# Optimization experiments

Hardware: AMD Instinct MI355X
Metric: run time of the kernel (lower is better)

The kernel has to match this reference:

```python
import jax, jax.numpy as jnp
import numpy as np

N_NODES = 100000
N_EDGES = 3200000
IN_DIM = 128
HID = 16
MEM = 16
N_LAYERS = 2
OUT = 2
SLOPE = 0.01  # torch leaky_relu default negative_slope


def setup_inputs() -> dict:
    key = jax.random.key(0)
    ks = jax.random.split(key, 20)
    s = 0.05
    inp = {
        "x": jax.random.normal(ks[0], (N_NODES, IN_DIM), dtype=jnp.float32),
        "edge_index": jax.random.randint(ks[1], (2, N_EDGES), 0, N_NODES, dtype=jnp.int64),
        # preprocess MLP: Linear(input_dim,256) -> Linear(256,hidden)
        "pre1_W": jax.random.normal(ks[2], (256, IN_DIM), dtype=jnp.float32) * s,
        "pre1_b": jax.random.normal(ks[3], (256,), dtype=jnp.float32) * s,
        "pre2_W": jax.random.normal(ks[4], (HID, 256), dtype=jnp.float32) * s,
        "pre2_b": jax.random.normal(ks[5], (HID,), dtype=jnp.float32) * s,
        # per-layer hypernetwork GRU biases (input & initial hidden are zeros, so
        # only biases affect the GRU step) and weight_transform Linear(mem, hid*hid)
        "gru_bih": jax.random.normal(ks[6], (N_LAYERS, 3 * MEM), dtype=jnp.float32) * s,
        "gru_bhh": jax.random.normal(ks[7], (N_LAYERS, 3 * MEM), dtype=jnp.float32) * s,
        "wt_W": jax.random.normal(ks[8], (N_LAYERS, HID * HID, MEM), dtype=jnp.float32) * s,
        "wt_b": jax.random.normal(ks[9], (N_LAYERS, HID * HID), dtype=jnp.float32) * s,
        # GCNConv bias (kept as its own parameter in PyG; lin has bias=False)
        "gcn_b": jax.random.normal(ks[10], (N_LAYERS, HID), dtype=jnp.float32) * s,
        # postprocess heads
        "post1_W": jax.random.normal(ks[11], (OUT, HID), dtype=jnp.float32) * s,
        "post1_b": jax.random.normal(ks[12], (OUT,), dtype=jnp.float32) * s,
        "posta_W": jax.random.normal(ks[13], (1, HID), dtype=jnp.float32) * s,
        "posta_b": jax.random.normal(ks[14], (1,), dtype=jnp.float32) * s,
    }
    return inp


def _hyper_gcn_weight(bih, bhh, wt_W, wt_b):
    # GRU single step with zero input and zero initial hidden state:
    # only the biases contribute.  h' = (1-z)*n + z*h_prev, h_prev = 0.
    r = jax.nn.sigmoid(bih[:MEM] + bhh[:MEM])
    z = jax.nn.sigmoid(bih[MEM:2 * MEM] + bhh[MEM:2 * MEM])
    n = jnp.tanh(bih[2 * MEM:] + r * bhh[2 * MEM:])
    mem = (1.0 - z) * n  # [MEM]
    # weight_transform Linear -> view as lin.weight [out, in]; detached in torch
    W = (wt_W @ mem + wt_b).reshape(HID, HID)
    return jax.lax.stop_gradient(W)


def reference(x, edge_index, pre1_W, pre1_b, pre2_W, pre2_b, gru_bih, gru_bhh,
              wt_W, wt_b, gcn_b, post1_W, post1_b, posta_W, posta_b):
    N = x.shape[0]
    # preprocess (dropout p=0.0 -> identity)
    h = jax.nn.leaky_relu(x @ pre1_W.T + pre1_b, negative_slope=SLOPE)
    h = jax.nn.leaky_relu(h @ pre2_W.T + pre2_b, negative_slope=SLOPE)

    # GCN normalization with self-loops (PyG gcn_norm)
    src, dst = edge_index[0], edge_index[1]
    loops = jnp.arange(N, dtype=src.dtype)
    s = jnp.concatenate([src, loops])
    d = jnp.concatenate([dst, loops])
    deg = jax.ops.segment_sum(jnp.ones_like(d, dtype=h.dtype), d, num_segments=N)
    dinv = jnp.where(deg > 0, jax.lax.rsqrt(deg), 0.0)
    norm = dinv[s] * dinv[d]  # [E+N]

    for l in range(N_LAYERS):
        W = _hyper_gcn_weight(gru_bih[l], gru_bhh[l], wt_W[l], wt_b[l])
        xw = h @ W.T                                   # [N, HID]
        msg = xw[s] * norm[:, None]                    # gather + scale
        h = jax.ops.segment_sum(msg, d, num_segments=N) + gcn_b[l]
        h = jax.nn.leaky_relu(h, negative_slope=SLOPE)

    out = jnp.sum(h @ post1_W.T + post1_b, axis=-1)          # [N]
    anomaly = (h @ posta_W.T + posta_b)[:, 0]                # [N]
    return out, anomaly, h
```

## Files before the change

### kernel.cpp

```cpp
#include <hip/hip_runtime.h>
#include <hip/hip_bf16.h>
#include <math.h>

#define IN_DIM 128
#define PRE_HID 256
#define HID 16

__device__ __forceinline__ float lrelu(float v) { return v > 0.f ? v : 0.01f * v; }
__device__ __forceinline__ float fin(float v) { return (v == v && fabsf(v) < 1e30f) ? v : 0.f; }

__device__ __forceinline__ float ldp(const void* p, size_t i, int f32) {
    if (f32) return ((const float*)p)[i];
    unsigned u = ((const unsigned short*)p)[i];
    return __uint_as_float(u << 16);
}
__device__ __forceinline__ unsigned short f2bf(float f) {
    union { __hip_bfloat16 b; unsigned short u; } cv;
    cv.b = __float2bfloat16(f);
    return cv.u;
}
__device__ __forceinline__ void unpack8(uint4 u, float* o) {
    o[0] = __uint_as_float(u.x << 16); o[1] = __uint_as_float(u.x & 0xFFFF0000u);
    o[2] = __uint_as_float(u.y << 16); o[3] = __uint_as_float(u.y & 0xFFFF0000u);
    o[4] = __uint_as_float(u.z << 16); o[5] = __uint_as_float(u.z & 0xFFFF0000u);
    o[6] = __uint_as_float(u.w << 16); o[7] = __uint_as_float(u.w & 0xFFFF0000u);
}
__device__ __forceinline__ unsigned pk2(float a, float b) {
    return (unsigned)f2bf(a) | ((unsigned)f2bf(b) << 16);
}
__device__ __forceinline__ uint4 pack8(const float* v) {
    uint4 u;
    u.x = pk2(v[0], v[1]); u.y = pk2(v[2], v[3]);
    u.z = pk2(v[4], v[5]); u.w = pk2(v[6], v[7]);
    return u;
}

#define OFF_W1F   0
#define OFF_B1F   32768
#define OFF_W2T   33024
#define OFF_B2F   37120
#define OFF_HW    37136
#define OFF_GCNB  37648
#define OFF_POST  37680
#define OFF_FLAGS 37720
#define OFF_BSUM  37760
#define OFF_BPRE  37888
#define OFF_A0    38016

__global__ void k_detect(const unsigned short* __restrict__ xu,
                         const int* __restrict__ ei32, int* __restrict__ flags) {
    if (threadIdx.x == 0 && blockIdx.x == 0) {
        int band = 0;
        for (int k = 0; k < 128; ++k) {
            unsigned e = (xu[2 * k] >> 7) & 0xFF;
            if (e >= 100 && e <= 140) band++;
        }
        flags[1] = (band < 96) ? 1 : 0;
        int any = 0;
        for (int k = 0; k < 64; ++k) any |= ei32[2 * k + 1];
        flags[0] = (any == 0) ? 1 : 0;
    }
}

__global__ void k_sentinel(unsigned* __restrict__ out, int words, unsigned val) {
    int i = blockIdx.x * 256 + threadIdx.x;
    if (i < words) out[i] = val;
}

__global__ void k_prep_small(const void* __restrict__ bih, const void* __restrict__ bhh,
                             const void* __restrict__ wtW, const void* __restrict__ wtb,
                             const void* __restrict__ p1W, const void* __restrict__ p1b,
                             const void* __restrict__ paW, const void* __restrict__ pab,
                             const int* __restrict__ flags,
                             float* __restrict__ hw, float* __restrict__ post) {
    int f32 = flags[1];
    __shared__ float mem[2][16];
    int t = threadIdx.x;
    if (t < 32) {
        int l = t >> 4, j = t & 15;
        float bi0 = ldp(bih, l * 48 + j, f32),      bh0 = ldp(bhh, l * 48 + j, f32);
        float bi1 = ldp(bih, l * 48 + 16 + j, f32), bh1 = ldp(bhh, l * 48 + 16 + j, f32);
        float bi2 = ldp(bih, l * 48 + 32 + j, f32), bh2 = ldp(bhh, l * 48 + 32 + j, f32);
        float r = 1.f / (1.f + expf(-(bi0 + bh0)));
        float z = 1.f / (1.f + expf(-(bi1 + bh1)));
        float nn = tanhf(bi2 + r * bh2);
        mem[l][j] = (1.f - z) * nn;
    }
    __syncthreads();
    for (int l = 0; l < 2; ++l) {
        float acc = ldp(wtb, l * 256 + t, f32);
        #pragma unroll
        for (int m = 0; m < 16; ++m)
            acc += ldp(wtW, l * 4096 + t * 16 + m, f32) * mem[l][m];
        hw[l * 256 + t] = acc;
    }
    if (t < 16) {
        post[t]      = ldp(p1W, t, f32) + ldp(p1W, 16 + t, f32);
        post[17 + t] = ldp(paW, t, f32);
    }
    if (t == 0) {
        post[16] = ldp(p1b, 0, f32) + ldp(p1b, 1, f32);
        post[33] = ldp(pab, 0, f32);
    }
}

__global__ void k_convert(const void* __restrict__ p1W, const void* __restrict__ p1b,
                          const void* __restrict__ p2W, const void* __restrict__ p2b,
                          const void* __restrict__ gcnb, const int* __restrict__ flags,
                          float* __restrict__ w1f, float* __restrict__ b1f,
                          float* __restrict__ w2t, float* __restrict__ b2f,
                          float* __restrict__ gcnbf) {
    int f32 = flags[1];
    int i = blockIdx.x * 256 + threadIdx.x;
    if (i < 32768) w1f[i] = ldp(p1W, i, f32);
    if (i < 256)   b1f[i] = ldp(p1b, i, f32);
    if (i < 4096)  { int r = i >> 4, j = i & 15; w2t[i] = ldp(p2W, j * 256 + r, f32); }
    if (i < 16)    b2f[i] = ldp(p2b, i, f32);
    if (i < 32)    gcnbf[i] = ldp(gcnb, i, f32);
}

__global__ void k_deg(const int* __restrict__ ei, const int* __restrict__ flags,
                      unsigned* __restrict__ deg, int E, int N) {
    int e = blockIdx.x * 256 + threadIdx.x;
    if (e >= E) return;
    int d = flags[0] ? ei[2 * ((size_t)E + e)] : ei[(size_t)E + e];
    if ((unsigned)d < (unsigned)N) atomicAdd(&deg[d], 1u);
}

__global__ void k_dinv(float* __restrict__ degdinv, int N) {
    int n = blockIdx.x * 256 + threadIdx.x;
    if (n >= N) return;
    unsigned dg = ((unsigned*)degdinv)[n];
    degdinv[n] = 1.f / sqrtf((float)dg + 1.f);
}

__global__ void k_dinv2(const unsigned* __restrict__ deg, float* __restrict__ dinv, int N) {
    int n = blockIdx.x * 256 + threadIdx.x;
    if (n >= N) return;
    dinv[n] = 1.f / sqrtf((float)deg[n] + 1.f);
}

__global__ __launch_bounds__(1024) void k_scan_block(const unsigned* __restrict__ deg,
                                                     unsigned* __restrict__ bsum, int N) {
    __shared__ unsigned s[1024];
    int t = threadIdx.x;
    int i = blockIdx.x * 1024 + t;
    s[t] = (i < N) ? deg[i] : 0u;
    __syncthreads();
    for (int off = 512; off > 0; off >>= 1) {
        if (t < off) s[t] += s[t + off];
        __syncthreads();
    }
    if (t == 0) bsum[blockIdx.x] = s[0];
}

__global__ __launch_bounds__(128) void k_scan_top(unsigned* __restrict__ bsum,
                                                  unsigned* __restrict__ bpre, int NB) {
    __shared__ unsigned s[128];
    int t = threadIdx.x;
    unsigned v = (t < NB) ? bsum[t] : 0u;
    s[t] = v;
    __syncthreads();
    for (int off = 1; off < 128; off <<= 1) {
        unsigned a = (t >= off) ? s[t - off] : 0u;
        __syncthreads();
        s[t] += a;
        __syncthreads();
    }
    if (t < NB) bpre[t] = s[t] - v;
}

__global__ __launch_bounds__(1024) void k_scan_final(const unsigned* __restrict__ deg,
                                                     const unsigned* __restrict__ bpre,
                                                     unsigned* __restrict__ rowptr, int N) {
    __shared__ unsigned s[1024];
    int t = threadIdx.x;
    int i = blockIdx.x * 1024 + t;
    unsigned v = (i < N) ? deg[i] : 0u;
    s[t] = v;
    __syncthreads();
    for (int off = 1; off < 1024; off <<= 1) {
        unsigned a = (t >= off) ? s[t - off] : 0u;
        __syncthreads();
        s[t] += a;
        __syncthreads();
    }
    if (i < N) rowptr[i] = bpre[blockIdx.x] + s[t] - v;
}

__global__ void k_fill(const int* __restrict__ ei, const int* __restrict__ flags,
                       unsigned* __restrict__ rowptr, unsigned* __restrict__ csr,
                       int E, int N) {
    int e = blockIdx.x * 256 + threadIdx.x;
    if (e >= E) return;
    int s, d;
    if (flags[0]) { s = ei[2 * (size_t)e]; d = ei[2 * ((size_t)E + e)]; }
    else          { s = ei[e];             d = ei[(size_t)E + e]; }
    if ((unsigned)d >= (unsigned)N) return;
    if ((unsigned)s >= (unsigned)N) s = d;
    unsigned pos = atomicAdd(&rowptr[d], 1u);
    csr[pos] = (unsigned)s;
}

__global__ __launch_bounds__(256) void k_pre(const void* __restrict__ x,
                                             const float* __restrict__ w1f,
                                             const float* __restrict__ b1f,
                                             const float* __restrict__ w2t,
                                             const float* __restrict__ b2f,
                                             const int* __restrict__ flags,
                                             float* __restrict__ h, int N) {
    int n = blockIdx.x * 256 + threadIdx.x;
    if (n >= N) return;
    float xr[IN_DIM];
    if (flags[1]) {
        const float4* xp = reinterpret_cast<const float4*>((const float*)x + (size_t)n * IN_DIM);
        #pragma unroll
        for (int i = 0; i < 32; ++i) {
            float4 v = xp[i];
            xr[i * 4 + 0] = v.x; xr[i * 4 + 1] = v.y; xr[i * 4 + 2] = v.z; xr[i * 4 + 3] = v.w;
        }
    } else {
        const uint4* xp = reinterpret_cast<const uint4*>((const unsigned short*)x + (size_t)n * IN_DIM);
        #pragma unroll
        for (int i = 0; i < 16; ++i) unpack8(xp[i], xr + i * 8);
    }
    float acc2[HID];
    #pragma unroll
    for (int j = 0; j < HID; ++j) acc2[j] = b2f[j];
    for (int r = 0; r < PRE_HID; ++r) {
        float s = b1f[r];
        const float* wr = w1f + r * IN_DIM;
        #pragma unroll
        for (int k = 0; k < IN_DIM; ++k) s += wr[k] * xr[k];
        s = lrelu(s);
        const float* w2r = w2t + r * HID;
        #pragma unroll
        for (int j = 0; j < HID; ++j) acc2[j] += w2r[j] * s;
    }
    float4* hp = reinterpret_cast<float4*>(h + (size_t)n * HID);
    #pragma unroll
    for (int q = 0; q < 4; ++q) {
        float4 v;
        v.x = lrelu(acc2[q * 4 + 0]); v.y = lrelu(acc2[q * 4 + 1]);
        v.z = lrelu(acc2[q * 4 + 2]); v.w = lrelu(acc2[q * 4 + 3]);
        hp[q] = v;
    }
}

__global__ void k_xw_y(const float* __restrict__ h, const float* __restrict__ W,
                       const float* __restrict__ dinv, float* __restrict__ y, int N) {
    int n = blockIdx.x * 256 + threadIdx.x;
    if (n >= N) return;
    float hv[HID];
    const float4* hp = reinterpret_cast<const float4*>(h + (size_t)n * HID);
    #pragma unroll
    for (int q = 0; q < 4; ++q) {
        float4 v = hp[q];
        hv[q*4+0] = v.x; hv[q*4+1] = v.y; hv[q*4+2] = v.z; hv[q*4+3] = v.w;
    }
    float dn = dinv[n];
    float4* yp = reinterpret_cast<float4*>(y + (size_t)n * HID);
    #pragma unroll
    for (int q = 0; q < 4; ++q) {
        float o[4];
        #pragma unroll
        for (int ii = 0; ii < 4; ++ii) {
            int i = q * 4 + ii;
            float s = 0.f;
            #pragma unroll
            for (int j = 0; j < HID; ++j) s += W[i * HID + j] * hv[j];
            o[ii] = s * dn;
        }
        float4 v; v.x = o[0]; v.y = o[1]; v.z = o[2]; v.w = o[3];
        yp[q] = v;
    }
}

__global__ __launch_bounds__(256) void k_gather(const unsigned* __restrict__ rowptr,
                                                const unsigned* __restrict__ deg,
                                                const unsigned* __restrict__ csr,
                                                const float* __restrict__ y,
                                                const float* __restrict__ dinv,
                                                const float* __restrict__ gcnbf,
                                                float* __restrict__ h, int N) {
    int tid = blockIdx.x * 256 + threadIdx.x;
    if (tid >= N * HID) return;
    int n = tid >> 4, f = tid & 15;
    unsigned end = rowptr[n];
    unsigned start = end - deg[n];
    float acc = y[(size_t)n * HID + f];
    for (unsigned k = start; k < end; ++k) {
        unsigned src = csr[k];
        acc += y[(size_t)src * HID + f];
    }
    h[(size_t)n * HID + f] = lrelu(fin(dinv[n] * acc) + gcnbf[f]);
}

__global__ __launch_bounds__(256) void k_gather_final(const unsigned* __restrict__ rowptr,
                                                      const unsigned* __restrict__ deg,
                                                      const unsigned* __restrict__ csr,
                                                      const float* __restrict__ y,
                                                      const float* __restrict__ dinv,
                                                      const float* __restrict__ gcnbf,
                                                      const float* __restrict__ post,
                                                      const int* __restrict__ flags,
                                                      void* __restrict__ out, int N) {
    int tid = blockIdx.x * 256 + threadIdx.x;
    if (tid >= N * HID) return;
    int n = tid >> 4, f = tid & 15;
    unsigned end = rowptr[n];
    unsigned start = end - deg[n];
    float acc = y[(size_t)n * HID + f];
    for (unsigned k = start; k < end; ++k) {
        unsigned src = csr[k];
        acc += y[(size_t)src * HID + f];
    }
    float v = lrelu(fin(dinv[n] * acc) + gcnbf[f]);
    float s1 = v * post[f];
    float s2 = v * post[17 + f];
    #pragma unroll
    for (int m = 1; m < 16; m <<= 1) {
        s1 += __shfl_xor(s1, m, 64);
        s2 += __shfl_xor(s2, m, 64);
    }
    if (flags[1]) {
        float* ob = (float*)out;
        if (f == 0) ob[n] = s1 + post[16];
        if (f == 1) ob[N + n] = s2 + post[33];
        ob[2 * (size_t)N + (size_t)n * HID + f] = v;
    } else {
        unsigned short* ob = (unsigned short*)out;
        if (f == 0) ob[n] = f2bf(s1 + post[16]);
        if (f == 1) ob[N + n] = f2bf(s2 + post[33]);
        ob[2 * (size_t)N + (size_t)n * HID + f] = f2bf(v);
    }
}

__global__ void k_xw(const float* __restrict__ h, const float* __restrict__ W,
                     const float* __restrict__ dinv, const int* __restrict__ flags,
                     void* __restrict__ xw, float* __restrict__ hacc, int N) {
    int n = blockIdx.x * 256 + threadIdx.x;
    if (n >= N) return;
    float hv[HID];
    const float4* hp = reinterpret_cast<const float4*>(h + (size_t)n * HID);
    #pragma unroll
    for (int q = 0; q < 4; ++q) {
        float4 v = hp[q];
        hv[q*4+0] = v.x; hv[q*4+1] = v.y; hv[q*4+2] = v.z; hv[q*4+3] = v.w;
    }
    float dn = dinv[n];
    float sl = dn * dn;
    float o[HID];
    #pragma unroll
    for (int i = 0; i < HID; ++i) {
        float s = 0.f;
        #pragma unroll
        for (int j = 0; j < HID; ++j) s += W[i * HID + j] * hv[j];
        o[i] = s;
    }
    if (flags[1]) {
        float4* xp = reinterpret_cast<float4*>((float*)xw + (size_t)n * HID);
        #pragma unroll
        for (int q = 0; q < 4; ++q) {
            float4 v; v.x = o[q*4+0]; v.y = o[q*4+1]; v.z = o[q*4+2]; v.w = o[q*4+3];
            xp[q] = v;
        }
    } else {
        uint4* xp = reinterpret_cast<uint4*>((unsigned short*)xw + (size_t)n * HID);
        xp[0] = pack8(o);
        xp[1] = pack8(o + 8);
    }
    float4* ap = reinterpret_cast<float4*>(hacc + (size_t)n * HID);
    #pragma unroll
    for (int q = 0; q < 4; ++q) {
        float4 va;
        va.x = o[q*4+0]*sl; va.y = o[q*4+1]*sl; va.z = o[q*4+2]*sl; va.w = o[q*4+3]*sl;
        ap[q] = va;
    }
}

__global__ __launch_bounds__(256) void k_scatter(const int* __restrict__ ei,
                                                 const int* __restrict__ flags,
                                                 const float* __restrict__ dinv,
                                                 const void* __restrict__ xw,
                                                 float* __restrict__ hacc, int E, int N) {
    int e = blockIdx.x * 256 + threadIdx.x;
    if (e >= E) return;
    int s, d;
    if (flags[0]) { s = ei[2 * (size_t)e]; d = ei[2 * ((size_t)E + e)]; }
    else          { s = ei[e];             d = ei[(size_t)E + e]; }
    if ((unsigned)s >= (unsigned)N || (unsigned)d >= (unsigned)N) return;
    float nrm = dinv[s] * dinv[d];
    float v[HID];
    if (flags[1]) {
        const float4* xr = reinterpret_cast<const float4*>((const float*)xw + (size_t)s * HID);
        #pragma unroll
        for (int q = 0; q < 4; ++q) {
            float4 a = xr[q];
            v[q*4+0] = a.x; v[q*4+1] = a.y; v[q*4+2] = a.z; v[q*4+3] = a.w;
        }
    } else {
        const uint4* xr = reinterpret_cast<const uint4*>((const unsigned short*)xw + (size_t)s * HID);
        unpack8(xr[0], v);
        unpack8(xr[1], v + 8);
    }
    float* out = hacc + (size_t)d * HID;
    #pragma unroll
    for (int j = 0; j < HID; ++j) unsafeAtomicAdd(out + j, v[j] * nrm);
}

__global__ void k_finish(const float* __restrict__ hacc, const float* __restrict__ gcnbf,
                         float* __restrict__ h, int N) {
    int n = blockIdx.x * 256 + threadIdx.x;
    if (n >= N) return;
    const float4* ap = reinterpret_cast<const float4*>(hacc + (size_t)n * HID);
    float4* hp = reinterpret_cast<float4*>(h + (size_t)n * HID);
    #pragma unroll
    for (int q = 0; q < 4; ++q) {
        float4 a = ap[q];
        float4 o;
        o.x = lrelu(fin(a.x) + gcnbf[q*4+0]);
        o.y = lrelu(fin(a.y) + gcnbf[q*4+1]);
        o.z = lrelu(fin(a.z) + gcnbf[q*4+2]);
        o.w = lrelu(fin(a.w) + gcnbf[q*4+3]);
        hp[q] = o;
    }
}

__global__ void k_final(const float* __restrict__ hacc, const float* __restrict__ gcnbf,
                        const float* __restrict__ post, const int* __restrict__ flags,
                        void* __restrict__ out, int N) {
    int n = blockIdx.x * 256 + threadIdx.x;
    if (n >= N) return;
    float v[HID];
    const float4* ap = reinterpret_cast<const float4*>(hacc + (size_t)n * HID);
    #pragma unroll
    for (int q = 0; q < 4; ++q) {
        float4 a = ap[q];
        v[q*4+0] = lrelu(fin(a.x) + gcnbf[q*4+0]);
        v[q*4+1] = lrelu(fin(a.y) + gcnbf[q*4+1]);
        v[q*4+2] = lrelu(fin(a.z) + gcnbf[q*4+2]);
        v[q*4+3] = lrelu(fin(a.w) + gcnbf[q*4+3]);
    }
    float o = post[16], an = post[33];
    #pragma unroll
    for (int j = 0; j < HID; ++j) {
        o += v[j] * post[j];
        an += v[j] * post[17 + j];
    }
    if (flags[1]) {
        float* ob = (float*)out;
        ob[n] = o;
        ob[N + n] = an;
        float* hr = ob + 2 * (size_t)N + (size_t)n * HID;
        #pragma unroll
        for (int j = 0; j < HID; ++j) hr[j] = v[j];
    } else {
        unsigned short* ob = (unsigned short*)out;
        ob[n] = f2bf(o);
        ob[N + n] = f2bf(an);
        uint4* hr = reinterpret_cast<uint4*>(ob + 2 * (size_t)N + (size_t)n * HID);
        hr[0] = pack8(v);
        hr[1] = pack8(v + 8);
    }
}

extern "C" void kernel_launch(void* const* d_in, const int* in_sizes, int n_in,
                              void* d_out, int out_size, void* d_ws, size_t ws_size,
                              hipStream_t stream) {
    const void* x    = d_in[0];
    const int*  ei   = (const int*)d_in[1];
    const void* p1W  = d_in[2];
    const void* p1b  = d_in[3];
    const void* p2W  = d_in[4];
    const void* p2b  = d_in[5];
    const void* bih  = d_in[6];
    const void* bhh  = d_in[7];
    const void* wtW  = d_in[8];
    const void* wtb  = d_in[9];
    const void* gcnb = d_in[10];
    const void* po1W = d_in[11];
    const void* po1b = d_in[12];
    const void* poaW = d_in[13];
    const void* poab = d_in[14];

    const int N = in_sizes[0] / IN_DIM;
    const int E = in_sizes[1] / 2;

    float* ws = (float*)d_ws;
    float* w1f   = ws + OFF_W1F;
    float* b1f   = ws + OFF_B1F;
    float* w2t   = ws + OFF_W2T;
    float* b2f   = ws + OFF_B2F;
    float* hw    = ws + OFF_HW;
    float* gcnbf = ws + OFF_GCNB;
    float* post  = ws + OFF_POST;
    int*   flags = (int*)(ws + OFF_FLAGS);
    unsigned* bsum = (unsigned*)(ws + OFF_BSUM);
    unsigned* bpre = (unsigned*)(ws + OFF_BPRE);

    const int nb_nodes = (N + 255) / 256;
    const int nb_edges = (E + 255) / 256;
    const int nb_nf    = (N * HID + 255) / 256;
    const int NB       = (N + 1023) / 1024;

    size_t req_csr = ((size_t)OFF_A0 + 35 * (size_t)N + (size_t)E + 64) * 4;
    size_t req_fb  = ((size_t)OFF_A0 + 33 * (size_t)N + 64) * 4;

    if (ws_size >= req_csr && NB <= 128) {
        unsigned* deg    = (unsigned*)(ws + OFF_A0);
        unsigned* rowptr = deg + N;
        float*    dinv   = (float*)(rowptr + N);
        unsigned* csr    = (unsigned*)(dinv + N);
        float*    y      = (float*)(csr + E);
        float*    h      = y + (size_t)N * HID;

        hipMemsetAsync(deg, 0, (size_t)N * 4, stream);
        k_detect<<<1, 64, 0, stream>>>((const unsigned short*)x, ei, flags);
        k_prep_small<<<1, 256, 0, stream>>>(bih, bhh, wtW, wtb, po1W, po1b, poaW, poab,
                                            flags, hw, post);
        k_convert<<<128, 256, 0, stream>>>(p1W, p1b, p2W, p2b, gcnb, flags,
                                           w1f, b1f, w2t, b2f, gcnbf);
        k_deg<<<nb_edges, 256, 0, stream>>>(ei, flags, deg, E, N);
        k_dinv2<<<nb_nodes, 256, 0, stream>>>(deg, dinv, N);
        k_scan_block<<<NB, 1024, 0, stream>>>(deg, bsum, N);
        k_scan_top<<<1, 128, 0, stream>>>(bsum, bpre, NB);
        k_scan_final<<<NB, 1024, 0, stream>>>(deg, bpre, rowptr, N);
        k_fill<<<nb_edges, 256, 0, stream>>>(ei, flags, rowptr, csr, E, N);
        k_pre<<<nb_nodes, 256, 0, stream>>>(x, w1f, b1f, w2t, b2f, flags, h, N);

        k_xw_y<<<nb_nodes, 256, 0, stream>>>(h, hw + 0, dinv, y, N);
        k_gather<<<nb_nf, 256, 0, stream>>>(rowptr, deg, csr, y, dinv, gcnbf + 0, h, N);
        k_xw_y<<<nb_nodes, 256, 0, stream>>>(h, hw + 256, dinv, y, N);
        k_gather_final<<<nb_nf, 256, 0, stream>>>(rowptr, deg, csr, y, dinv, gcnbf + 16,
                                                  post, flags, d_out, N);
    } else if (ws_size >= req_fb) {
        float* degdinv = ws + OFF_A0;
        float* hacc    = degdinv + N;
        float* h       = hacc + (size_t)N * HID;
        void*  xw      = d_out;

        hipMemsetAsync(degdinv, 0, (size_t)N * 4, stream);
        k_detect<<<1, 64, 0, stream>>>((const unsigned short*)x, ei, flags);
        k_prep_small<<<1, 256, 0, stream>>>(bih, bhh, wtW, wtb, po1W, po1b, poaW, poab,
                                            flags, hw, post);
        k_convert<<<128, 256, 0, stream>>>(p1W, p1b, p2W, p2b, gcnb, flags,
                                           w1f, b1f, w2t, b2f, gcnbf);
        k_deg<<<nb_edges, 256, 0, stream>>>(ei, flags, (unsigned*)degdinv, E, N);
        k_dinv<<<nb_nodes, 256, 0, stream>>>(degdinv, N);
        k_pre<<<nb_nodes, 256, 0, stream>>>(x, w1f, b1f, w2t, b2f, flags, h, N);
        for (int l = 0; l < 2; ++l) {
            k_xw<<<nb_nodes, 256, 0, stream>>>(h, hw + l * 256, degdinv, flags, xw, hacc, N);
            k_scatter<<<nb_edges, 256, 0, stream>>>(ei, flags, degdinv, xw, hacc, E, N);
            if (l == 0) k_finish<<<nb_nodes, 256, 0, stream>>>(hacc, gcnbf + 0, h, N);
            else        k_final<<<nb_nodes, 256, 0, stream>>>(hacc, gcnbf + 16, post, flags, d_out, N);
        }
    } else {
        float f = 256.0f + (float)(ws_size >> 20);
        unsigned uv; __builtin_memcpy(&uv, &f, 4);
        int words = out_size / 2;
        k_sentinel<<<(words + 255) / 256, 256, 0, stream>>>((unsigned*)d_out, words, uv);
    }
}
```

Before: 1.085 ms.

## Tile preprocess MLP over hidden rows and vectorize CSR gathers with float4

The preprocess kernel no longer holds a 128-float input row in registers. It walks 32-row tiles of the first layer and streams the input in chunks of 8, keeping 32 partial sums, which is meant to cut register pressure and raise occupancy. The gather kernels now use 4 threads per node, each loading float4 slices, instead of 16 scalar threads. This cuts per-edge loads of CSR indices and row pointers by a factor of four but gives fewer threads per node. The input is now re-read 8 times from cache in the preprocess kernel.

```diff
diff --git a/kernel.cpp b/kernel.cpp
--- a/kernel.cpp
+++ b/kernel.cpp
@@ -211,31 +211,45 @@
                                              float* __restrict__ h, int N) {
     int n = blockIdx.x * 256 + threadIdx.x;
     if (n >= N) return;
-    float xr[IN_DIM];
-    if (flags[1]) {
-        const float4* xp = reinterpret_cast<const float4*>((const float*)x + (size_t)n * IN_DIM);
-        #pragma unroll
-        for (int i = 0; i < 32; ++i) {
-            float4 v = xp[i];
-            xr[i * 4 + 0] = v.x; xr[i * 4 + 1] = v.y; xr[i * 4 + 2] = v.z; xr[i * 4 + 3] = v.w;
-        }
-    } else {
-        const uint4* xp = reinterpret_cast<const uint4*>((const unsigned short*)x + (size_t)n * IN_DIM);
-        #pragma unroll
-        for (int i = 0; i < 16; ++i) unpack8(xp[i], xr + i * 8);
-    }
+    const int f32 = flags[1];
+    const float* xf = (const float*)x + (size_t)n * IN_DIM;
+    const unsigned short* xb = (const unsigned short*)x + (size_t)n * IN_DIM;
+
     float acc2[HID];
     #pragma unroll
     for (int j = 0; j < HID; ++j) acc2[j] = b2f[j];
-    for (int r = 0; r < PRE_HID; ++r) {
-        float s = b1f[r];
-        const float* wr = w1f + r * IN_DIM;
-        #pragma unroll
-        for (int k = 0; k < IN_DIM; ++k) s += wr[k] * xr[k];
-        s = lrelu(s);
-        const float* w2r = w2t + r * HID;
-        #pragma unroll
-        for (int j = 0; j < HID; ++j) acc2[j] += w2r[j] * s;
+
+    for (int rt = 0; rt < 8; ++rt) {
+        float s[32];
+        #pragma unroll
+        for (int r = 0; r < 32; ++r) s[r] = b1f[rt * 32 + r];
+        for (int kc = 0; kc < 16; ++kc) {
+            float xr[8];
+            if (f32) {
+                float4 a = *reinterpret_cast<const float4*>(xf + kc * 8);
+                float4 b = *reinterpret_cast<const float4*>(xf + kc * 8 + 4);
+                xr[0] = a.x; xr[1] = a.y; xr[2] = a.z; xr[3] = a.w;
+                xr[4] = b.x; xr[5] = b.y; xr[6] = b.z; xr[7] = b.w;
+            } else {
+                uint4 u = *reinterpret_cast<const uint4*>(xb + kc * 8);
+                unpack8(u, xr);
+            }
+            const float* wbase = w1f + (size_t)(rt * 32) * IN_DIM + kc * 8;
+            #pragma unroll
+            for (int r = 0; r < 32; ++r) {
+                const float* wr = wbase + (size_t)r * IN_DIM;
+                #pragma unroll
+                for (int k = 0; k < 8; ++k) s[r] += wr[k] * xr[k];
+            }
+        }
+        const float* w2base = w2t + (size_t)(rt * 32) * HID;
+        #pragma unroll
+        for (int r = 0; r < 32; ++r) {
+            float t = lrelu(s[r]);
+            const float* w2r = w2base + (size_t)r * HID;
+            #pragma unroll
+            for (int j = 0; j < HID; ++j) acc2[j] += w2r[j] * t;
+        }
     }
     float4* hp = reinterpret_cast<float4*>(h + (size_t)n * HID);
     #pragma unroll
@@ -284,16 +298,23 @@
                                                 const float* __restrict__ gcnbf,
                                                 float* __restrict__ h, int N) {
     int tid = blockIdx.x * 256 + threadIdx.x;
-    if (tid >= N * HID) return;
-    int n = tid >> 4, f = tid & 15;
+    if (tid >= N * 4) return;
+    int n = tid >> 2, q = tid & 3;
     unsigned end = rowptr[n];
     unsigned start = end - deg[n];
-    float acc = y[(size_t)n * HID + f];
+    float4 acc = *reinterpret_cast<const float4*>(y + (size_t)n * HID + q * 4);
     for (unsigned k = start; k < end; ++k) {
         unsigned src = csr[k];
-        acc += y[(size_t)src * HID + f];
-    }
-    h[(size_t)n * HID + f] = lrelu(fin(dinv[n] * acc) + gcnbf[f]);
+        float4 v = *reinterpret_cast<const float4*>(y + (size_t)src * HID + q * 4);
+        acc.x += v.x; acc.y += v.y; acc.z += v.z; acc.w += v.w;
+    }
+    float dn = dinv[n];
+    float4 o;
+    o.x = lrelu(fin(dn * acc.x) + gcnbf[q*4+0]);
+    o.y = lrelu(fin(dn * acc.y) + gcnbf[q*4+1]);
+    o.z = lrelu(fin(dn * acc.z) + gcnbf[q*4+2]);
+    o.w = lrelu(fin(dn * acc.w) + gcnbf[q*4+3]);
+    *reinterpret_cast<float4*>(h + (size_t)n * HID + q * 4) = o;
 }
 
 __global__ __launch_bounds__(256) void k_gather_final(const unsigned* __restrict__ rowptr,
@@ -306,33 +327,40 @@
                                                       const int* __restrict__ flags,
                                                       void* __restrict__ out, int N) {
     int tid = blockIdx.x * 256 + threadIdx.x;
-    if (tid >= N * HID) return;
-    int n = tid >> 4, f = tid & 15;
+    if (tid >= N * 4) return;
+    int n = tid >> 2, q = tid & 3;
     unsigned end = rowptr[n];
     unsigned start = end - deg[n];
-    float acc = y[(size_t)n * HID + f];
+    float4 acc = *reinterpret_cast<const float4*>(y + (size_t)n * HID + q * 4);
     for (unsigned k = start; k < end; ++k) {
         unsigned src = csr[k];
-        acc += y[(size_t)src * HID + f];
-    }
-    float v = lrelu(fin(dinv[n] * acc) + gcnbf[f]);
-    float s1 = v * post[f];
-    float s2 = v * post[17 + f];
-    #pragma unroll
-    for (int m = 1; m < 16; m <<= 1) {
+        float4 v = *reinterpret_cast<const float4*>(y + (size_t)src * HID + q * 4);
+        acc.x += v.x; acc.y += v.y; acc.z += v.z; acc.w += v.w;
+    }
+    float dn = dinv[n];
+    float v0 = lrelu(fin(dn * acc.x) + gcnbf[q*4+0]);
+    float v1 = lrelu(fin(dn * acc.y) + gcnbf[q*4+1]);
+    float v2 = lrelu(fin(dn * acc.z) + gcnbf[q*4+2]);
+    float v3 = lrelu(fin(dn * acc.w) + gcnbf[q*4+3]);
+    float s1 = v0 * post[q*4+0] + v1 * post[q*4+1] + v2 * post[q*4+2] + v3 * post[q*4+3];
+    float s2 = v0 * post[17+q*4+0] + v1 * post[17+q*4+1] + v2 * post[17+q*4+2] + v3 * post[17+q*4+3];
+    #pragma unroll
+    for (int m = 1; m < 4; m <<= 1) {
         s1 += __shfl_xor(s1, m, 64);
         s2 += __shfl_xor(s2, m, 64);
     }
     if (flags[1]) {
         float* ob = (float*)out;
-        if (f == 0) ob[n] = s1 + post[16];
-        if (f == 1) ob[N + n] = s2 + post[33];
-        ob[2 * (size_t)N + (size_t)n * HID + f] = v;
+        if (q == 0) ob[n] = s1 + post[16];
+        if (q == 1) ob[N + n] = s2 + post[33];
+        float4 o; o.x = v0; o.y = v1; o.z = v2; o.w = v3;
+        *reinterpret_cast<float4*>(ob + 2 * (size_t)N + (size_t)n * HID + q * 4) = o;
     } else {
         unsigned short* ob = (unsigned short*)out;
-        if (f == 0) ob[n] = f2bf(s1 + post[16]);
-        if (f == 1) ob[N + n] = f2bf(s2 + post[33]);
-        ob[2 * (size_t)N + (size_t)n * HID + f] = f2bf(v);
+        if (q == 0) ob[n] = f2bf(s1 + post[16]);
+        if (q == 1) ob[N + n] = f2bf(s2 + post[33]);
+        uint2 u; u.x = pk2(v0, v1); u.y = pk2(v2, v3);
+        *reinterpret_cast<uint2*>(ob + 2 * (size_t)N + (size_t)n * HID + q * 4) = u;
     }
 }
 
@@ -501,7 +529,7 @@
 
     const int nb_nodes = (N + 255) / 256;
     const int nb_edges = (E + 255) / 256;
-    const int nb_nf    = (N * HID + 255) / 256;
+    const int nb_n4    = (N * 4 + 255) / 256;
     const int NB       = (N + 1023) / 1024;
 
     size_t req_csr = ((size_t)OFF_A0 + 35 * (size_t)N + (size_t)E + 64) * 4;
@@ -530,9 +558,9 @@
         k_pre<<<nb_nodes, 256, 0, stream>>>(x, w1f, b1f, w2t, b2f, flags, h, N);
 
         k_xw_y<<<nb_nodes, 256, 0, stream>>>(h, hw + 0, dinv, y, N);
-        k_gather<<<nb_nf, 256, 0, stream>>>(rowptr, deg, csr, y, dinv, gcnbf + 0, h, N);
+        k_gather<<<nb_n4, 256, 0, stream>>>(rowptr, deg, csr, y, dinv, gcnbf + 0, h, N);
         k_xw_y<<<nb_nodes, 256, 0, stream>>>(h, hw + 256, dinv, y, N);
-        k_gather_final<<<nb_nf, 256, 0, stream>>>(rowptr, deg, csr, y, dinv, gcnbf + 16,
+        k_gather_final<<<nb_n4, 256, 0, stream>>>(rowptr, deg, csr, y, dinv, gcnbf + 16,
                                                   post, flags, d_out, N);
     } else if (ws_size >= req_fb) {
         float* degdinv = ws + OFF_A0;
```

Result: faster. 979.4 us (-9.7%).
